# Performance work log

Hardware: AMD Instinct MI355X
Metric: run time of the kernel (lower is better)

Reference implementation:

```python
import jax, jax.numpy as jnp
import numpy as np
from jax import lax

B, S, E, H, V, L = 16, 256, 256, 256, 50000, 9


def setup_inputs() -> dict:
    key = jax.random.key(0)
    ks = jax.random.split(key, 12)
    s = 0.05
    return {
        "input_ids": jax.random.randint(ks[0], (B, S), 0, V),
        "attention_mask": jnp.ones((B, S), dtype=jnp.int32),
        "labels": jax.random.randint(ks[1], (B, S), 0, L),
        "embedding": jax.random.normal(ks[2], (V, E), jnp.float32) * s,
        "w_ih_l0": jax.random.normal(ks[3], (2, 4 * H, E), jnp.float32) * s,
        "w_ih_rest": jax.random.normal(ks[4], (3, 2, 4 * H, 2 * H), jnp.float32) * s,
        "w_hh": jax.random.normal(ks[5], (4, 2, 4 * H, H), jnp.float32) * s,
        "b": jax.random.normal(ks[6], (4, 2, 2, 4 * H), jnp.float32) * s,
        "ln_g": jnp.ones((2 * H,), jnp.float32),
        "ln_b": jnp.zeros((2 * H,), jnp.float32),
        "lin_w": jax.random.normal(ks[7], (L, 2 * H), jnp.float32) * s,
        "lin_b": jnp.zeros((L,), jnp.float32),
        "crf_start": jax.random.normal(ks[8], (L,), jnp.float32) * s,
        "crf_end": jax.random.normal(ks[9], (L,), jnp.float32) * s,
        "crf_trans": jax.random.normal(ks[10], (L, L), jnp.float32) * s,
    }


def _lstm_dir(x, w_ih, w_hh, b_ih, b_hh, reverse):
    # x: [B,S,in]; PyTorch gate order i,f,g,o packed along 4H.
    Bb = x.shape[0]
    Hh = w_hh.shape[1]
    xg = jnp.einsum('bsi,gi->bsg', x, w_ih) + b_ih + b_hh  # precompute input projection
    if reverse:
        xg = xg[:, ::-1]

    def step(carry, g):
        h, c = carry
        g = g + h @ w_hh.T
        i, f, gg, o = jnp.split(g, 4, axis=-1)
        c = jax.nn.sigmoid(f) * c + jax.nn.sigmoid(i) * jnp.tanh(gg)
        h = jax.nn.sigmoid(o) * jnp.tanh(c)
        return (h, c), h

    z = jnp.zeros((Bb, Hh), x.dtype)
    _, hs = lax.scan(step, (z, z), jnp.swapaxes(xg, 0, 1))
    hs = jnp.swapaxes(hs, 0, 1)  # [B,S,H]
    if reverse:
        hs = hs[:, ::-1]
    return hs


def _forward(input_ids, attention_mask, labels, embedding, w_ih_l0, w_ih_rest,
             w_hh, b, ln_g, ln_b, lin_w, lin_b, crf_start, crf_end, crf_trans):
    x = embedding[input_ids]  # [B,S,E]
    for layer in range(4):
        wf = w_ih_l0[0] if layer == 0 else w_ih_rest[layer - 1, 0]
        wb = w_ih_l0[1] if layer == 0 else w_ih_rest[layer - 1, 1]
        hf = _lstm_dir(x, wf, w_hh[layer, 0], b[layer, 0, 0], b[layer, 0, 1], False)
        hb = _lstm_dir(x, wb, w_hh[layer, 1], b[layer, 1, 0], b[layer, 1, 1], True)
        x = jnp.concatenate([hf, hb], axis=-1)  # [B,S,2H]
    # dropout is identity in eval mode
    mu = x.mean(-1, keepdims=True)
    var = ((x - mu) ** 2).mean(-1, keepdims=True)
    x = (x - mu) * lax.rsqrt(var + 1e-5) * ln_g + ln_b
    logits = jnp.einsum('bsh,lh->bsl', x, lin_w) + lin_b  # emissions [B,S,L]

    # CRF negative log-likelihood (torchcrf semantics, reduction='sum')
    Bb = logits.shape[0]
    mask_f = attention_mask.astype(logits.dtype)
    bidx = jnp.arange(Bb)
    first = labels[:, 0]
    num = crf_start[first] + logits[bidx, 0, first]
    em_t = jnp.swapaxes(logits, 0, 1)[1:]  # [S-1,B,L]
    tprev = labels[:, :-1].T
    tcur = labels[:, 1:].T
    mt = mask_f[:, 1:].T

    def num_step(s, inp):
        e, tp, tc, m = inp
        return s + (crf_trans[tp, tc] + e[bidx, tc]) * m, None

    num, _ = lax.scan(num_step, num, (em_t, tprev, tcur, mt))
    last = jnp.sum(attention_mask, axis=1).astype(jnp.int32) - 1
    num = num + crf_end[labels[bidx, last]]

    alpha = crf_start + logits[:, 0]  # [B,L]

    def den_step(a, inp):
        e, m = inp
        nxt = jax.nn.logsumexp(a[:, :, None] + crf_trans[None] + e[:, None, :], axis=1)
        return jnp.where(m[:, None] > 0, nxt, a), None

    alpha, _ = lax.scan(den_step, alpha, (em_t, mt))
    denom = jax.nn.logsumexp(alpha + crf_end, axis=-1)
    loss = -(num - denom).sum()
    return logits, loss


def reference(input_ids, attention_mask, labels, embedding, w_ih_l0, w_ih_rest,
              w_hh, b, ln_g, ln_b, lin_w, lin_b, crf_start, crf_end, crf_trans):
    return _forward(input_ids, attention_mask, labels, embedding, w_ih_l0,
                    w_ih_rest, w_hh, b, ln_g, ln_b, lin_w, lin_b,
                    crf_start, crf_end, crf_trans)
```

## Files before the change

kernel.cpp:

```cpp
#include <hip/hip_runtime.h>
#include <math.h>
#include <stdint.h>

#define BB 16
#define SS 256
#define LL 9
#define ROWS 4096
#define HP 272

typedef __attribute__((ext_vector_type(8))) short short8;
typedef __attribute__((ext_vector_type(4))) float f32x4;
typedef __attribute__((ext_vector_type(8))) int i32x8;

#define HSCALE 256.0f
#define LOG2E  1.44269504f
#define WCONST 1477.3199f
#define SCALE_ONE 0x7F7F7F7Fu
#define SCALE_IFO 0x6D6D6D6Du
#define SCALE_G   0x6E6E6E6Eu

__device__ __forceinline__ unsigned short f2bf(float f) {
  unsigned u = __float_as_uint(f);
  return (unsigned short)((u + 0x7FFF + ((u >> 16) & 1)) >> 16);
}
__device__ __forceinline__ float bf2f(unsigned short s) {
  return __uint_as_float(((unsigned)s) << 16);
}

__device__ __forceinline__ void gl2lds16(const void* g, void* l) {
  __builtin_amdgcn_global_load_lds(
      (const __attribute__((address_space(1))) void*)g,
      (__attribute__((address_space(3))) void*)l, 16, 0, 0);
}

__device__ __forceinline__ void barrier_lds_only() {
  asm volatile("s_waitcnt lgkmcnt(0)" ::: "memory");
  __builtin_amdgcn_s_barrier();
  asm volatile("" ::: "memory");
}

__global__ __launch_bounds__(256) void prep_all(
    const int* __restrict__ ids, const float* __restrict__ emb,
    unsigned short* __restrict__ x0,
    const float* __restrict__ w_l0, const float* __restrict__ w_rest,
    unsigned short* __restrict__ wp,
    const float* __restrict__ whh, unsigned* __restrict__ wfrag,
    const float* __restrict__ b2, float* __restrict__ biasPF) {
  int bid = blockIdx.x;
  int tid = threadIdx.x;

  if (bid < 4096) {
    int id = ids[bid];
    x0[(size_t)bid * 256 + tid] = f2bf(emb[(size_t)id * 256 + tid]);
    return;
  }
  bid -= 4096;

  if (bid < 16384) {
    int l = bid >> 12;
    int bx = bid & 4095;
    int Ksh = l ? 9 : 8;
    int K = 1 << Ksh;
    long total = (long)2 * 1024 * K;
    long idx = (long)bx * 256 + tid;
    if (idx >= total) return;
    int k = (int)(idx & (K - 1));
    long r = idx >> Ksh;
    int np = (int)(r & 1023), dir = (int)(r >> 10);
    int nph = ((np & 3) << 8) + (np >> 2);
    float cg = ((np & 3) == 2) ? (2.0f * LOG2E) : (-LOG2E);
    const float* src = l ? (w_rest + (size_t)(l - 1) * 2 * 1024 * 512) : w_l0;
    size_t off = l ? (524288 + (size_t)(l - 1) * 1048576) : 0;
    wp[off + idx] = f2bf(src[((size_t)dir * 1024 + nph) * K + k] * cg);
    return;
  }
  bid -= 16384;

  if (bid < 256) {
    int u = bid * 4 + (tid >> 6);
    int lane = tid & 63;
    int z = u >> 7;
    int rr = u & 127;
    int ks2 = rr >> 6;
    int nb = rr & 63;
    int qq = lane >> 4, col = lane & 15;
    int g = nb >> 4;
    float csc = (g == 2) ? WCONST : -WCONST;
    const float* wpp = whh + (size_t)z * 1024 * 256 +
                       (size_t)(nb * 16 + col) * 256 + ks2 * 128 + qq * 32;
    unsigned* op = wfrag + (((size_t)(z * 64 + nb) * 2 + ks2) * 64 + lane) * 8;
#pragma unroll
    for (int uu = 0; uu < 8; ++uu) {
      float v0 = wpp[uu * 4 + 0] * csc, v1 = wpp[uu * 4 + 1] * csc;
      float v2 = wpp[uu * 4 + 2] * csc, v3 = wpp[uu * 4 + 3] * csc;
      unsigned pk = __builtin_amdgcn_cvt_pk_fp8_f32(v0, v1, 0, false);
      pk = __builtin_amdgcn_cvt_pk_fp8_f32(v2, v3, pk, true);
      op[uu] = pk;
    }
    return;
  }
  bid -= 256;

  int i = bid * 256 + tid;
  int l = i >> 11, r = i & 2047;
  int dir = r >> 10, np = r & 1023;
  int n = ((np & 3) << 8) + (np >> 2);
  float cg = ((np & 3) == 2) ? (2.0f * LOG2E) : (-LOG2E);
  biasPF[i] = (b2[l * 4096 + dir * 2048 + n] + b2[l * 4096 + dir * 2048 + 1024 + n]) * cg;
}

__global__ __launch_bounds__(512) void gemm_xg128(
    const unsigned short* __restrict__ A, int K,
    const unsigned short* __restrict__ BP,
    const float* __restrict__ biasPF,
    unsigned short* __restrict__ xgP) {
  int dir = blockIdx.z;
  int n0 = blockIdx.x * 128, m0 = blockIdx.y * 128;
  int tid = threadIdx.x;
  int wv = tid >> 6, lane = tid & 63, quad = lane >> 4, col = lane & 15;
  __shared__ unsigned short Ls[16384];
  const unsigned short* Bw = BP + (size_t)dir * 1024 * K;

  int srow = lane >> 2;
  int scol = (lane & 3) * 8;
  const unsigned short* ga = A + (size_t)(m0 + wv * 16 + srow) * K + scol;
  const unsigned short* gb = Bw + (size_t)(n0 + wv * 16 + srow) * K + scol;
  int lofs = wv * 512;

  int wm = wv & 1;
  int wn = wv >> 1;
  f32x4 acc[4][2];
#pragma unroll
  for (int mt = 0; mt < 4; ++mt)
#pragma unroll
    for (int nt = 0; nt < 2; ++nt) acc[mt][nt] = (f32x4){0.f, 0.f, 0.f, 0.f};

  int nIter = K >> 5;
  gl2lds16(ga, &Ls[lofs]);
  gl2lds16(gb, &Ls[8192 + lofs]);
  ga += 32; gb += 32;
  __syncthreads();

  for (int it = 0; it < nIter; ++it) {
    int cb = it & 1;
    if (it + 1 < nIter) {
      gl2lds16(ga, &Ls[(cb ^ 1) * 4096 + lofs]);
      gl2lds16(gb, &Ls[8192 + (cb ^ 1) * 4096 + lofs]);
      ga += 32; gb += 32;
    }
    const unsigned short* Ab = &Ls[cb * 4096];
    const unsigned short* Bb = &Ls[8192 + cb * 4096];
    short8 bf0 = *(const short8*)&Bb[(wn * 32 + col) * 32 + quad * 8];
    short8 bf1 = *(const short8*)&Bb[(wn * 32 + 16 + col) * 32 + quad * 8];
#pragma unroll
    for (int mt = 0; mt < 4; ++mt) {
      short8 af = *(const short8*)&Ab[(wm * 64 + mt * 16 + col) * 32 + quad * 8];
      acc[mt][0] = __builtin_amdgcn_mfma_f32_16x16x32_bf16(af, bf0, acc[mt][0], 0, 0, 0);
      acc[mt][1] = __builtin_amdgcn_mfma_f32_16x16x32_bf16(af, bf1, acc[mt][1], 0, 0, 0);
    }
    __syncthreads();
  }

#pragma unroll
  for (int nt = 0; nt < 2; ++nt) {
    int npl = wn * 32 + nt * 16 + col;
    float bia = biasPF[dir * 1024 + n0 + npl];
#pragma unroll
    for (int mt = 0; mt < 4; ++mt)
#pragma unroll
      for (int r = 0; r < 4; ++r)
        Ls[(wm * 64 + mt * 16 + quad * 4 + r) * 128 + npl] =
            f2bf(acc[mt][nt][r] + bia);
  }
  __syncthreads();
  unsigned short* od = xgP + (size_t)dir * ROWS * 1024;
#pragma unroll
  for (int it = 0; it < 4; ++it) {
    int e = (it * 512 + tid) * 8;
    int row = e >> 7, npl = e & 127;
    *(short8*)&od[(size_t)(m0 + row) * 1024 + n0 + npl] = *(const short8*)&Ls[e];
  }
}

__global__ __launch_bounds__(1024, 4) void lstm_mx(
    const unsigned short* __restrict__ xgP,
    const unsigned* __restrict__ wfrag,
    unsigned short* __restrict__ xout) {
  int dir = blockIdx.x & 1;
  int bg = blockIdx.x >> 1;
  int tid = threadIdx.x;
  int wv = tid >> 6, lane = tid & 63;
  int quad = lane >> 4, col = lane & 15;

  __shared__ __align__(16) unsigned char Hfrag[2][4 * HP];

  {
    int* hz = (int*)&Hfrag[0][0];
    for (int i = tid; i < HP; i += 1024) hz[i] = 0;
  }

  i32x8 wf[4][2];
#pragma unroll
  for (int g = 0; g < 4; ++g) {
    int nb = g * 16 + wv;
#pragma unroll
    for (int ks2 = 0; ks2 < 2; ++ks2)
      wf[g][ks2] = *(const i32x8*)(wfrag +
          (((size_t)(dir * 64 + nb) * 2 + ks2) * 64 + lane) * 8);
  }

  int aoff = ((lane & 15) >> 2) * HP + (lane >> 4) * 32;

  int j = 16 * wv + col;
  int b = bg * 4 + quad;
  int pos0 = dir ? (SS - 1) : 0;
  int dstep = dir ? -1 : 1;
  const unsigned short* xq_ptr =
      xgP + ((size_t)dir * ROWS + (size_t)b * SS + pos0) * 1024 + j * 4;
  unsigned short* xo_ptr = xout + ((size_t)b * SS + pos0) * 512 + dir * 256 + j;
  int xq_d = dstep * 1024;
  int xo_d = dstep * 512;
  int hw = quad * HP + j;

  float Cp = 0.f;
  int cur = 0;
  ushort4 xq_n = *(const ushort4*)xq_ptr;
  xq_ptr += xq_d;
  __syncthreads();

  for (int t = 0; t < SS; ++t) {
    ushort4 xq = xq_n;
    xq_n = *(const ushort4*)xq_ptr;
    xq_ptr += xq_d;

    i32x8 af0 = *(const i32x8*)&Hfrag[cur][aoff];
    i32x8 af1 = *(const i32x8*)&Hfrag[cur][aoff + 128];

    f32x4 acc[4];
    acc[0] = (f32x4){bf2f(xq.x), 0.f, 0.f, 0.f};
    acc[1] = (f32x4){bf2f(xq.y), 0.f, 0.f, 0.f};
    acc[2] = (f32x4){bf2f(xq.z), 0.f, 0.f, 0.f};
    acc[3] = (f32x4){bf2f(xq.w), 0.f, 0.f, 0.f};
#pragma unroll
    for (int g = 0; g < 4; ++g) {
      unsigned sb = (g == 2) ? SCALE_G : SCALE_IFO;
      acc[g] = __builtin_amdgcn_mfma_scale_f32_16x16x128_f8f6f4(
          af0, wf[g][0], acc[g], 0, 0, 0, SCALE_ONE, 0, sb);
      acc[g] = __builtin_amdgcn_mfma_scale_f32_16x16x128_f8f6f4(
          af1, wf[g][1], acc[g], 0, 0, 0, SCALE_ONE, 0, sb);
    }

    int nxt = cur ^ 1;
    float gi = acc[0][0];
    float gf = acc[1][0];
    float gt = acc[2][0];
    float go = acc[3][0];
    float si = __builtin_amdgcn_rcpf(1.0f + __builtin_amdgcn_exp2f(gi));
    float sf = __builtin_amdgcn_rcpf(1.0f + __builtin_amdgcn_exp2f(gf));
    float so = __builtin_amdgcn_rcpf(1.0f + __builtin_amdgcn_exp2f(go));
    float rg = __builtin_amdgcn_rcpf(1.0f + __builtin_amdgcn_exp2f(gt));
    float tg2 = fmaf(-4.0f * LOG2E, rg, 2.0f * LOG2E);
    Cp = fmaf(sf, Cp, si * tg2);
    float rc = __builtin_amdgcn_rcpf(1.0f + __builtin_amdgcn_exp2f(Cp));
    float h = so * fmaf(-2.0f, rc, 1.0f);

    unsigned pk = __builtin_amdgcn_cvt_pk_fp8_f32(h * HSCALE, h * HSCALE, 0, false);
    Hfrag[nxt][hw] = (unsigned char)(pk & 0xFF);
    *xo_ptr = f2bf(h);
    xo_ptr += xo_d;

    barrier_lds_only();
    cur = nxt;
  }
}

__global__ __launch_bounds__(256) void ln_logits(
    const unsigned short* __restrict__ X, const float* __restrict__ g,
    const float* __restrict__ bt, const float* __restrict__ W,
    const float* __restrict__ lb, float* __restrict__ out) {
  int row = blockIdx.x * 4 + (threadIdx.x >> 6);
  int lane = threadIdx.x & 63;
  const unsigned short* x = X + (size_t)row * 512;
  float v[8];
  float s = 0.f, s2 = 0.f;
#pragma unroll
  for (int i = 0; i < 8; ++i) {
    v[i] = bf2f(x[lane + 64 * i]);
    s += v[i];
    s2 += v[i] * v[i];
  }
#pragma unroll
  for (int off = 32; off; off >>= 1) {
    s += __shfl_down(s, off, 64);
    s2 += __shfl_down(s2, off, 64);
  }
  s = __shfl(s, 0, 64);
  s2 = __shfl(s2, 0, 64);
  float mu = s * (1.f / 512.f);
  float var = s2 * (1.f / 512.f) - mu * mu;
  float rstd = rsqrtf(var + 1e-5f);
  float y[8];
#pragma unroll
  for (int i = 0; i < 8; ++i) {
    int e = lane + 64 * i;
    y[i] = (v[i] - mu) * rstd * g[e] + bt[e];
  }
  for (int l = 0; l < LL; ++l) {
    float p = 0.f;
#pragma unroll
    for (int i = 0; i < 8; ++i) p += y[i] * W[(size_t)l * 512 + lane + 64 * i];
#pragma unroll
    for (int off = 32; off; off >>= 1) p += __shfl_down(p, off, 64);
    if (lane == 0) out[(size_t)row * LL + l] = p + lb[l];
  }
}

__global__ __launch_bounds__(256) void crf_kernel(
    const float* __restrict__ logits, const int* __restrict__ labels,
    const int* __restrict__ mask, const float* __restrict__ cs,
    const float* __restrict__ ce, const float* __restrict__ ct,
    float* __restrict__ loss_out) {
  __shared__ float trans[9][12];
  __shared__ float alpha[2][BB][12];
  __shared__ float numsh[BB];
  __shared__ float res[BB];
  int tid = threadIdx.x;
  int b = tid >> 4;
  int i = tid & 15;
  if (tid < 81) trans[tid / 9][tid % 9] = ct[tid];
  __syncthreads();
  const float* lg = logits + (size_t)b * SS * LL;
  const int* lbp = labels + (size_t)b * SS;
  const int* mk = mask + (size_t)b * SS;

  float np = 0.f;
  int msum = 0;
  for (int t = i; t < SS; t += 16) {
    msum += mk[t];
    if (t == 0) {
      int l0 = lbp[0];
      np += cs[l0] + lg[l0];
    } else {
      float m = (float)mk[t];
      np += (trans[lbp[t - 1]][lbp[t]] + lg[(size_t)t * LL + lbp[t]]) * m;
    }
  }
#pragma unroll
  for (int off = 8; off; off >>= 1) {
    np += __shfl_down(np, off, 16);
    msum += __shfl_down(msum, off, 16);
  }
  if (i == 0) {
    int last = msum - 1;
    numsh[b] = np + ce[lbp[last]];
  }

  if (i < LL) alpha[0][b][i] = cs[i] + lg[i];
  int cur = 0;
  for (int t = 1; t < SS; ++t) {
    if (i < LL) {
      float e = lg[(size_t)t * LL + i];
      float av[9];
      float mmax = -1e30f;
#pragma unroll
      for (int p = 0; p < LL; ++p) {
        float vv = alpha[cur][b][p] + trans[p][i];
        av[p] = vv;
        mmax = fmaxf(mmax, vv);
      }
      float ssum = 0.f;
#pragma unroll
      for (int p = 0; p < LL; ++p) ssum += __expf(av[p] - mmax);
      float anew = e + mmax + logf(ssum);
      float aold = alpha[cur][b][i];
      alpha[cur ^ 1][b][i] = (mk[t] > 0) ? anew : aold;
    }
    cur ^= 1;
  }
  if (i == 0) {
    float arr[9];
    float m2 = -1e30f;
#pragma unroll
    for (int cc = 0; cc < LL; ++cc) {
      arr[cc] = alpha[cur][b][cc] + ce[cc];
      m2 = fmaxf(m2, arr[cc]);
    }
    float ssd = 0.f;
#pragma unroll
    for (int cc = 0; cc < LL; ++cc) ssd += __expf(arr[cc] - m2);
    float denom = m2 + logf(ssd);
    res[b] = numsh[b] - denom;
  }
  __syncthreads();
  if (tid == 0) {
    float Lsum = 0.f;
    for (int b2 = 0; b2 < BB; ++b2) Lsum += res[b2];
    loss_out[0] = -Lsum;
  }
}

extern "C" void kernel_launch(void* const* d_in, const int* in_sizes, int n_in,
                              void* d_out, int out_size, void* d_ws, size_t ws_size,
                              hipStream_t stream) {
  const int* input_ids = (const int*)d_in[0];
  const int* attn_mask = (const int*)d_in[1];
  const int* labels = (const int*)d_in[2];
  const float* embedding = (const float*)d_in[3];
  const float* w_ih_l0 = (const float*)d_in[4];
  const float* w_ih_rest = (const float*)d_in[5];
  const float* w_hh = (const float*)d_in[6];
  const float* bvec = (const float*)d_in[7];
  const float* ln_g = (const float*)d_in[8];
  const float* ln_b = (const float*)d_in[9];
  const float* lin_w = (const float*)d_in[10];
  const float* lin_b = (const float*)d_in[11];
  const float* crf_start = (const float*)d_in[12];
  const float* crf_end = (const float*)d_in[13];
  const float* crf_trans = (const float*)d_in[14];
  float* out = (float*)d_out;
  char* base = (char*)d_ws;

  unsigned short* x0    = (unsigned short*)(base);
  unsigned short* xoutA = (unsigned short*)(base + (2u << 20));
  unsigned short* xoutB = (unsigned short*)(base + (6u << 20));
  unsigned short* xgP   = (unsigned short*)(base + (10u << 20));
  unsigned*       wfrag = (unsigned*)(base + (26u << 20));
  float*          biasPF= (float*)(base + (28u << 20));
  unsigned short* wihP  = (unsigned short*)(base + (29u << 20));

  prep_all<<<20768, 256, 0, stream>>>(input_ids, embedding, x0,
                                      w_ih_l0, w_ih_rest, wihP,
                                      w_hh, wfrag, bvec, biasPF);

  const size_t WOFF[4] = {0, 524288, 1572864, 2621440};

  const unsigned short* cur = x0;
  unsigned short* nxt = xoutA;
  for (int l = 0; l < 4; ++l) {
    int K = l ? 512 : 256;
    gemm_xg128<<<dim3(8, 32, 2), 512, 0, stream>>>(
        cur, K, wihP + WOFF[l], biasPF + (size_t)l * 2048, xgP);
    lstm_mx<<<8, 1024, 0, stream>>>(xgP, wfrag + (size_t)l * 131072, nxt);
    cur = nxt;
    nxt = (nxt == xoutA) ? xoutB : xoutA;
  }

  ln_logits<<<1024, 256, 0, stream>>>(cur, ln_g, ln_b, lin_w, lin_b, out);
  crf_kernel<<<1, 256, 0, stream>>>(out, labels, attn_mask, crf_start, crf_end,
                                    crf_trans, out + (size_t)ROWS * LL);
}
```

Before: 993.2 us.

## Run CRF forward recursion in scaled exp domain with shuffles instead of LDS

Rewrites the CRF partition-function recursion to keep alpha in the linear (exponentiated) domain with a running log-scale offset. Each step becomes a dot product against precomputed exp(trans) plus one exp, instead of a max, nine exps and a log. Alpha values are exchanged with wavefront shuffles instead of shared memory, which drops the LDS round trip. Rescaling by powers of two bounds overflow and underflow, at the cost of slightly different numerics and a reliance on the 16-lane shuffle group.

```diff
diff --git a/kernel.cpp b/kernel.cpp
--- a/kernel.cpp
+++ b/kernel.cpp
@@ -321,7 +321,6 @@
     const float* __restrict__ ce, const float* __restrict__ ct,
     float* __restrict__ loss_out) {
   __shared__ float trans[9][12];
-  __shared__ float alpha[2][BB][12];
   __shared__ float numsh[BB];
   __shared__ float res[BB];
   int tid = threadIdx.x;
@@ -355,42 +354,50 @@
     numsh[b] = np + ce[lbp[last]];
   }
 
-  if (i < LL) alpha[0][b][i] = cs[i] + lg[i];
-  int cur = 0;
+  int ii = (i < LL) ? i : 0;
+  float ETc[9];
+#pragma unroll
+  for (int p = 0; p < LL; ++p) ETc[p] = __expf(trans[p][ii]);
+
+  float own = cs[ii] + lg[ii];
+  float a[9];
+#pragma unroll
+  for (int p = 0; p < LL; ++p) a[p] = __shfl(own, p, 16);
+  float C = a[0];
+#pragma unroll
+  for (int p = 1; p < LL; ++p) C = fmaxf(C, a[p]);
+  float ownA = __expf(own - C);
+#pragma unroll
+  for (int p = 0; p < LL; ++p) a[p] = __expf(a[p] - C);
+
   for (int t = 1; t < SS; ++t) {
-    if (i < LL) {
-      float e = lg[(size_t)t * LL + i];
-      float av[9];
-      float mmax = -1e30f;
-#pragma unroll
-      for (int p = 0; p < LL; ++p) {
-        float vv = alpha[cur][b][p] + trans[p][i];
-        av[p] = vv;
-        mmax = fmaxf(mmax, vv);
-      }
-      float ssum = 0.f;
-#pragma unroll
-      for (int p = 0; p < LL; ++p) ssum += __expf(av[p] - mmax);
-      float anew = e + mmax + logf(ssum);
-      float aold = alpha[cur][b][i];
-      alpha[cur ^ 1][b][i] = (mk[t] > 0) ? anew : aold;
-    }
-    cur ^= 1;
-  }
-  if (i == 0) {
-    float arr[9];
-    float m2 = -1e30f;
-#pragma unroll
-    for (int cc = 0; cc < LL; ++cc) {
-      arr[cc] = alpha[cur][b][cc] + ce[cc];
-      m2 = fmaxf(m2, arr[cc]);
-    }
-    float ssd = 0.f;
-#pragma unroll
-    for (int cc = 0; cc < LL; ++cc) ssd += __expf(arr[cc] - m2);
-    float denom = m2 + logf(ssd);
-    res[b] = numsh[b] - denom;
-  }
+    float e = lg[(size_t)t * LL + ii];
+    float s = 0.f;
+#pragma unroll
+    for (int p = 0; p < LL; ++p) s = fmaf(a[p], ETc[p], s);
+    float an = __expf(e) * s;
+    float ow = (mk[t] > 0) ? an : ownA;
+    float na[9];
+#pragma unroll
+    for (int p = 0; p < LL; ++p) na[p] = __shfl(ow, p, 16);
+    float M = na[0];
+#pragma unroll
+    for (int p = 1; p < LL; ++p) M = fmaxf(M, na[p]);
+    float f = 1.0f, dC = 0.0f;
+    if (M > 0x1p64f)       { f = 0x1p-64f; dC = 44.3614195558f; }
+    else if (M < 0x1p-32f) { f = 0x1p64f;  dC = -44.3614195558f; }
+    C += dC;
+#pragma unroll
+    for (int p = 0; p < LL; ++p) a[p] = na[p] * f;
+    ownA = ow * f;
+  }
+
+  float sd = 0.f;
+#pragma unroll
+  for (int p = 0; p < LL; ++p) sd = fmaf(a[p], __expf(ce[p]), sd);
+  float denom = C + __logf(sd);
+  if (i == 0) res[b] = numsh[b] - denom;
+
   __syncthreads();
   if (tid == 0) {
     float Lsum = 0.f;
```

Measured after the change: 985.5 us. No clear change (-0.8%).
